# Kernel optimization log

Measured on AMD Instinct MI355X. Metric: run time of the kernel, lower is better.

## Reference

```python
import jax, jax.numpy as jnp
import numpy as np

EMB_DIM = 2048
NHEADS = 16
KVHEADS = 4
D_KQ = 128
D_V = 128


def setup_inputs() -> dict:
    key = jax.random.key(0)
    ks = jax.random.split(key, 7)
    B, S = 2, 2048
    std = 0.02
    return {
        "q": jax.random.normal(ks[0], (B, S, EMB_DIM), jnp.float32),
        "k": jax.random.normal(ks[1], (B, S, EMB_DIM), jnp.float32),
        "v": jax.random.normal(ks[2], (B, S, EMB_DIM), jnp.float32),
        # weights stored [in, out] (transposed vs torch nn.Linear storage)
        "Wq": jax.random.normal(ks[3], (EMB_DIM, NHEADS * D_KQ), jnp.float32) * std,
        "Wk": jax.random.normal(ks[4], (EMB_DIM, KVHEADS * D_KQ), jnp.float32) * std,
        "Wv": jax.random.normal(ks[5], (EMB_DIM, KVHEADS * D_V), jnp.float32) * std,
        "Wo": jax.random.normal(ks[6], (NHEADS * D_V, EMB_DIM), jnp.float32) * std,
    }


def reference(q, k, v, Wq, Wk, Wv, Wo):
    B, S, _ = q.shape
    scale = D_KQ ** -0.25  # applied to both q and k -> combined 1/sqrt(d_kq)
    # per-head projections: [B, H, S, d]
    qh = (q @ Wq).reshape(B, S, NHEADS, D_KQ).transpose(0, 2, 1, 3) * scale
    kh = (k @ Wk).reshape(B, S, KVHEADS, D_KQ).transpose(0, 2, 1, 3) * scale
    vh = (v @ Wv).reshape(B, S, KVHEADS, D_V).transpose(0, 2, 1, 3)
    # GQA expansion: each kv head repeated `expansion` times consecutively
    expansion = NHEADS // KVHEADS
    kh = jnp.repeat(kh, expansion, axis=1)  # [B, H, S, d_kq]
    vh = jnp.repeat(vh, expansion, axis=1)  # [B, H, S, d_v]
    # full softmax FIRST, then causal tril mask, then renormalize (source quirk)
    scores = jax.nn.softmax(jnp.einsum("bhqd,bhkd->bhqk", qh, kh), axis=-1)
    scores = jnp.tril(scores)  # zero out strictly-upper triangle on last 2 dims
    scores = scores / (jnp.sum(scores, axis=-1, keepdims=True) + 1e-9)
    qkv = jnp.einsum("bhqk,bhkd->bhqd", scores, vh)  # [B, H, S, d_v]
    z = qkv.transpose(0, 2, 1, 3).reshape(B, S, NHEADS * D_V)
    return z @ Wo
```

## Files before the change

### kernel.cpp

```cpp
#include <hip/hip_runtime.h>

#define S_LEN 2048
#define EMB 2048
#define NH 16
#define KVH 4
#define DH 128

typedef __bf16 bf16x8 __attribute__((ext_vector_type(8)));
typedef float floatx4 __attribute__((ext_vector_type(4)));
typedef unsigned short ushortx8 __attribute__((ext_vector_type(8)));
typedef unsigned short ushortx4 __attribute__((ext_vector_type(4)));

static __device__ __forceinline__ unsigned short f2bf(float f) {
  unsigned u = __float_as_uint(f);
  return (unsigned short)((u + 0x7fffu + ((u >> 16) & 1u)) >> 16);
}

static __device__ __forceinline__ void gload16(const unsigned short* g, unsigned short* l) {
  __builtin_amdgcn_global_load_lds(
      (const __attribute__((address_space(1))) unsigned int*)(const void*)g,
      (__attribute__((address_space(3))) unsigned int*)(void*)l, 16, 0, 0);
}

__global__ __launch_bounds__(256) void pre_kernel(
    const float* __restrict__ q, const float* __restrict__ k, const float* __restrict__ v,
    const float* __restrict__ Wq, const float* __restrict__ Wk,
    const float* __restrict__ Wv, const float* __restrict__ Wo,
    unsigned short* __restrict__ qo, unsigned short* __restrict__ ko,
    unsigned short* __restrict__ vo,
    unsigned short* __restrict__ Wqt, unsigned short* __restrict__ Wkt,
    unsigned short* __restrict__ Wvt, unsigned short* __restrict__ Wot,
    float scale) {
  __shared__ float t[32][33];
  int bx = blockIdx.x;
  if (bx < 12288) {
    const int sel = bx >> 12;
    const float* in = (sel == 0) ? q : (sel == 1) ? k : v;
    unsigned short* out = (sel == 0) ? qo : (sel == 1) ? ko : vo;
    size_t i = (((size_t)(bx & 4095)) * 256 + threadIdx.x) * 8;
    floatx4 a = *(const floatx4*)(in + i);
    floatx4 bvec = *(const floatx4*)(in + i + 4);
    ushortx8 o;
    #pragma unroll
    for (int c = 0; c < 4; ++c) { o[c] = f2bf(a[c]); o[4 + c] = f2bf(bvec[c]); }
    *(ushortx8*)(out + i) = o;
  } else {
    bx -= 12288;
    const float* W; unsigned short* Wt; int N, tile; float sc;
    if (bx < 4096)      { W = Wq; Wt = Wqt; N = 2048; tile = bx;        sc = scale; }
    else if (bx < 5120) { W = Wk; Wt = Wkt; N = 512;  tile = bx - 4096; sc = scale; }
    else if (bx < 6144) { W = Wv; Wt = Wvt; N = 512;  tile = bx - 5120; sc = 1.0f; }
    else                { W = Wo; Wt = Wot; N = 2048; tile = bx - 6144; sc = 1.0f; }
    const int ntiles = N >> 5;
    const int n0 = (tile % ntiles) * 32, k0 = (tile / ntiles) * 32;
    const int tx = threadIdx.x & 31, ty = threadIdx.x >> 5;
    #pragma unroll
    for (int r = 0; r < 4; ++r)
      t[ty + r * 8][tx] = W[(size_t)(k0 + ty + r * 8) * N + n0 + tx];
    __syncthreads();
    #pragma unroll
    for (int r = 0; r < 4; ++r)
      Wt[(size_t)(n0 + ty + r * 8) * 2048 + k0 + tx] = f2bf(t[tx][ty + r * 8] * sc);
  }
}

static __device__ __forceinline__ void gemm256_core(
    const unsigned short* __restrict__ Ab, const unsigned short* __restrict__ Bb,
    bool swap, unsigned short* As, unsigned short* Bs, floatx4 (&acc)[8][4]) {
  const int tid = threadIdx.x;
  const int lane = tid & 63, w = tid >> 6;
  const int lm = lane & 15, gq = lane >> 4;
  const int wm = w >> 2, wn = w & 3;
  const int lr = lane >> 3, lc = (lane & 7) ^ lr;

  auto stageH = [&](const unsigned short* gb, unsigned short* lt, int half, int kst) {
    #pragma unroll
    for (int qq = 0; qq < 2; ++qq) {
      const int rb = half * 128 + w * 16 + qq * 8;
      gload16(gb + (((size_t)(rb + lr)) << 11) + kst + (lc << 3), lt + rb * 64);
    }
  };

  unsigned short* As2 = As + 16384;
  unsigned short* Bs2 = Bs + 16384;

  stageH(Ab, As, 0, 0);  stageH(Ab, As, 1, 0);
  stageH(Bb, Bs, 0, 0);  stageH(Bb, Bs, 1, 0);
  stageH(Ab, As2, 0, 64);
  asm volatile("s_waitcnt vmcnt(2)" ::: "memory");
  __builtin_amdgcn_s_barrier();

  const int r1 = (wm * 128 + lm) * 64;
  const int r2 = (wn * 64 + lm) * 64;
  const int c0 = ((0 + gq) ^ (lm & 7)) * 8;
  const int c1 = ((4 + gq) ^ (lm & 7)) * 8;

#define TILE_BODY(CA, CB, OA, OB, KS1, KS2, STG1, STG4)                                         \
  {                                                                                             \
    const unsigned short* l1 = swap ? (CB) : (CA);                                              \
    const unsigned short* l2 = swap ? (CA) : (CB);                                              \
    bf16x8 op1[8], o2a[4], o2b[4];                                                              \
    _Pragma("unroll") for (int i = 0; i < 8; ++i)                                               \
      op1[i] = *(const bf16x8*)&l1[r1 + i * 1024 + c0];                                         \
    _Pragma("unroll") for (int j = 0; j < 4; ++j)                                               \
      o2a[j] = *(const bf16x8*)&l2[r2 + j * 1024 + c0];                                         \
    if (STG1) stageH(Ab, (OA), 1, (KS1));                                                       \
    __builtin_amdgcn_s_barrier();                                                               \
    asm volatile("s_waitcnt lgkmcnt(0)" ::: "memory");                                          \
    __builtin_amdgcn_s_setprio(1);                                                              \
    _Pragma("unroll") for (int i = 0; i < 8; ++i) {                                             \
      acc[i][0] = __builtin_amdgcn_mfma_f32_16x16x32_bf16(op1[i], o2a[0], acc[i][0], 0, 0, 0);  \
      acc[i][1] = __builtin_amdgcn_mfma_f32_16x16x32_bf16(op1[i], o2a[1], acc[i][1], 0, 0, 0);  \
    }                                                                                           \
    __builtin_amdgcn_s_setprio(0);                                                              \
    __builtin_amdgcn_s_barrier();                                                               \
    _Pragma("unroll") for (int j = 0; j < 4; ++j)                                               \
      o2b[j] = *(const bf16x8*)&l2[r2 + j * 1024 + c1];                                         \
    if (STG1) stageH(Bb, (OB), 0, (KS1));                                                       \
    __builtin_amdgcn_s_barrier();                                                               \
    asm volatile("s_waitcnt lgkmcnt(0)" ::: "memory");                                          \
    __builtin_amdgcn_s_setprio(1);                                                              \
    _Pragma("unroll") for (int i = 0; i < 8; ++i) {                                             \
      acc[i][2] = __builtin_amdgcn_mfma_f32_16x16x32_bf16(op1[i], o2a[2], acc[i][2], 0, 0, 0);  \
      acc[i][3] = __builtin_amdgcn_mfma_f32_16x16x32_bf16(op1[i], o2a[3], acc[i][3], 0, 0, 0);  \
    }                                                                                           \
    __builtin_amdgcn_s_setprio(0);                                                              \
    __builtin_amdgcn_s_barrier();                                                               \
    _Pragma("unroll") for (int i = 0; i < 8; ++i)                                               \
      op1[i] = *(const bf16x8*)&l1[r1 + i * 1024 + c1];                                         \
    if (STG1) stageH(Bb, (OB), 1, (KS1));                                                       \
    __builtin_amdgcn_s_barrier();                                                               \
    asm volatile("s_waitcnt lgkmcnt(0)" ::: "memory");                                          \
    __builtin_amdgcn_s_setprio(1);                                                              \
    _Pragma("unroll") for (int i = 0; i < 8; ++i) {                                             \
      acc[i][0] = __builtin_amdgcn_mfma_f32_16x16x32_bf16(op1[i], o2b[0], acc[i][0], 0, 0, 0);  \
      acc[i][1] = __builtin_amdgcn_mfma_f32_16x16x32_bf16(op1[i], o2b[1], acc[i][1], 0, 0, 0);  \
    }                                                                                           \
    __builtin_amdgcn_s_setprio(0);                                                              \
    __builtin_amdgcn_s_barrier();                                                               \
    if (STG4) stageH(Ab, (CA), 0, (KS2));                                                       \
    __builtin_amdgcn_s_barrier();                                                               \
    __builtin_amdgcn_s_setprio(1);                                                              \
    _Pragma("unroll") for (int i = 0; i < 8; ++i) {                                             \
      acc[i][2] = __builtin_amdgcn_mfma_f32_16x16x32_bf16(op1[i], o2b[2], acc[i][2], 0, 0, 0);  \
      acc[i][3] = __builtin_amdgcn_mfma_f32_16x16x32_bf16(op1[i], o2b[3], acc[i][3], 0, 0, 0);  \
    }                                                                                           \
    __builtin_amdgcn_s_setprio(0);                                                              \
    if (STG4) { asm volatile("s_waitcnt vmcnt(2)" ::: "memory"); }                              \
    else      { asm volatile("s_waitcnt vmcnt(0)" ::: "memory"); }                              \
    __builtin_amdgcn_s_barrier();                                                               \
  }

  #pragma unroll 1
  for (int t = 0; t < 30; t += 2) {
    TILE_BODY(As, Bs, As2, Bs2, (t + 1) * 64, (t + 2) * 64, 1, 1);
    TILE_BODY(As2, Bs2, As, Bs, (t + 2) * 64, (t + 3) * 64, 1, 1);
  }
  TILE_BODY(As, Bs, As2, Bs2, 31 * 64, 0, 1, 0);
  TILE_BODY(As2, Bs2, As, Bs, 0, 0, 0, 0);
#undef TILE_BODY
}

__global__ __launch_bounds__(512, 2) void proj_kernel(
    const unsigned short* __restrict__ qb, const unsigned short* __restrict__ kb,
    const unsigned short* __restrict__ vb,
    const unsigned short* __restrict__ Wqt, const unsigned short* __restrict__ Wkt,
    const unsigned short* __restrict__ Wvt,
    unsigned short* __restrict__ Qh, unsigned short* __restrict__ Kh,
    unsigned short* __restrict__ Vt) {
  extern __shared__ unsigned short lds[];
  unsigned short* As = lds;
  unsigned short* Bs = lds + 32768;
  int bid = (int)blockIdx.x;
  bid = (bid & 7) * 24 + (bid >> 3);
  const unsigned short *Ab, *Bb;
  int task, bn, bt;
  if (bid < 128)      { task = 0; bn = bid >> 4;         bt = bid & 15;         Ab = qb; Bb = Wqt; }
  else if (bid < 160) { task = 1; bn = (bid - 128) >> 4; bt = (bid - 128) & 15; Ab = kb; Bb = Wkt; }
  else                { task = 2; bn = (bid - 160) >> 4; bt = (bid - 160) & 15; Ab = vb; Bb = Wvt; }
  Ab += ((size_t)bt) << 19;
  Bb += ((size_t)bn) << 19;

  floatx4 acc[8][4] = {};
  gemm256_core(Ab, Bb, task != 2, As, Bs, acc);

  const int tid = threadIdx.x, lane = tid & 63, w = tid >> 6;
  const int lm = lane & 15, gq = lane >> 4;
  const int wm = w >> 2, wn = w & 3;
  if (task != 2) {
    unsigned short* outp = (task == 0) ? Qh : Kh;
    const int nheads = (task == 0) ? NH : KVH;
    const int head = bn * 2 + wm;
    #pragma unroll
    for (int i = 0; i < 8; ++i) {
      const int d0 = i * 16 + gq * 4;
      #pragma unroll
      for (int j = 0; j < 4; ++j) {
        const int tg = bt * 256 + wn * 64 + j * 16 + lm;
        const int b_ = tg >> 11, s_ = tg & 2047;
        ushortx4 pk;
        #pragma unroll
        for (int r = 0; r < 4; ++r) pk[r] = f2bf(acc[i][j][r]);
        *(ushortx4*)&outp[((size_t)(b_ * nheads + head) * S_LEN + s_) * DH + d0] = pk;
      }
    }
  } else {
    #pragma unroll
    for (int i = 0; i < 8; ++i) {
      const int sgl = bt * 256 + wm * 128 + i * 16 + gq * 4;
      const int b_ = sgl >> 11, s_ = sgl & 2047;
      #pragma unroll
      for (int j = 0; j < 4; ++j) {
        const int dl = wn * 64 + j * 16;
        const int head = bn * 2 + (dl >> 7);
        const int dd = (dl & 127) + lm;
        ushortx4 pk;
        #pragma unroll
        for (int r = 0; r < 4; ++r) pk[r] = f2bf(acc[i][j][r]);
        *(ushortx4*)&Vt[((size_t)(b_ * KVH + head) * DH + dd) * S_LEN + s_] = pk;
      }
    }
  }
}

__global__ __launch_bounds__(512, 2) void out_kernel(const unsigned short* __restrict__ Z,
                                                     const unsigned short* __restrict__ Wot,
                                                     float* __restrict__ outp) {
  extern __shared__ unsigned short lds[];
  unsigned short* As = lds;
  unsigned short* Bs = lds + 32768;
  int bid = (int)blockIdx.x;
  bid = (bid & 7) * 16 + (bid >> 3);
  const int bn = bid >> 4, bt = bid & 15;

  floatx4 acc[8][4] = {};
  gemm256_core(Z + (((size_t)bt) << 19), Wot + (((size_t)bn) << 19), true, As, Bs, acc);

  const int tid = threadIdx.x, lane = tid & 63, w = tid >> 6;
  const int lm = lane & 15, gq = lane >> 4;
  const int wm = w >> 2, wn = w & 3;
  #pragma unroll
  for (int i = 0; i < 8; ++i) {
    const int n0 = bn * 256 + wm * 128 + i * 16 + gq * 4;
    #pragma unroll
    for (int j = 0; j < 4; ++j) {
      const int tg = bt * 256 + wn * 64 + j * 16 + lm;
      *(floatx4*)&outp[(size_t)tg * 2048 + n0] = acc[i][j];
    }
  }
}

__global__ __launch_bounds__(256) void attn_kernel(const unsigned short* __restrict__ Qh,
                                                   const unsigned short* __restrict__ Kh,
                                                   const unsigned short* __restrict__ Vt,
                                                   unsigned short* __restrict__ Z) {
  __shared__ unsigned short Ks[64][136];
  __shared__ unsigned short Vs[128][72];
  __shared__ unsigned short Ps[4][16][88];
  const int tid = threadIdx.x;
  const int w = tid >> 6, lane = tid & 63;
  const int lm = lane & 15, gq = lane >> 4;
  const int h = blockIdx.y, b = blockIdx.z;
  const unsigned short* Kp = Kh + (size_t)(b * KVH + (h >> 2)) * S_LEN * DH;
  const unsigned short* Vp = Vt + (size_t)(b * KVH + (h >> 2)) * DH * S_LEN;

  const int krow = tid >> 2, kq4 = tid & 3;
  const int vd = tid >> 1, vhf = tid & 1;

  ushortx8 kreg[4], vreg[4];
  {
    const unsigned short* ks = Kp + (size_t)krow * DH + kq4 * 32;
    const unsigned short* vs = Vp + (size_t)vd * S_LEN + vhf * 32;
    #pragma unroll
    for (int i = 0; i < 4; ++i) { kreg[i] = *(const ushortx8*)(ks + i * 8); vreg[i] = *(const ushortx8*)(vs + i * 8); }
  }

  bf16x8 ones;
  #pragma unroll
  for (int c = 0; c < 8; ++c) ones[c] = (__bf16)1.0f;

  #pragma unroll 1
  for (int pass = 0; pass < 2; ++pass) {
    const int qt = pass ? (int)blockIdx.x : 31 - (int)blockIdx.x;
    const int Q0 = qt * 64;
    const unsigned short* Qp = Qh + ((size_t)(b * NH + h) * S_LEN + Q0) * DH;
    bf16x8 qfr[4];
    #pragma unroll
    for (int kk = 0; kk < 4; ++kk)
      qfr[kk] = *(const bf16x8*)(Qp + (size_t)(w * 16 + lm) * DH + kk * 32 + gq * 8);

    floatx4 acc_o[8] = {};
    floatx4 acc_l = {};

    for (int it = 0; it <= qt; ++it) {
      const int kv0 = it * 64;
      __syncthreads();
      #pragma unroll
      for (int i = 0; i < 4; ++i) *(ushortx8*)&Ks[krow][kq4 * 32 + i * 8] = kreg[i];
      #pragma unroll
      for (int i = 0; i < 4; ++i) *(ushortx8*)&Vs[vd][vhf * 32 + i * 8] = vreg[i];
      __syncthreads();
      if (!(pass == 1 && it == qt)) {
        const int kvn = (it < qt) ? kv0 + 64 : 0;
        const unsigned short* ks = Kp + (size_t)(kvn + krow) * DH + kq4 * 32;
        const unsigned short* vs = Vp + (size_t)vd * S_LEN + kvn + vhf * 32;
        #pragma unroll
        for (int i = 0; i < 4; ++i) { kreg[i] = *(const ushortx8*)(ks + i * 8); vreg[i] = *(const ushortx8*)(vs + i * 8); }
      }
      floatx4 sa[4] = {};
      #pragma unroll
      for (int j = 0; j < 4; ++j)
        #pragma unroll
        for (int kk = 0; kk < 4; ++kk) {
          bf16x8 bk = *(const bf16x8*)&Ks[j * 16 + lm][kk * 32 + gq * 8];
          sa[j] = __builtin_amdgcn_mfma_f32_16x16x32_bf16(qfr[kk], bk, sa[j], 0, 0, 0);
        }
      const int rowb = Q0 + w * 16 + gq * 4;
      #pragma unroll
      for (int r = 0; r < 4; ++r) {
        const int qg = rowb + r;
        #pragma unroll
        for (int j = 0; j < 4; ++j) {
          const int kg = kv0 + j * 16 + lm;
          const float p = (kg <= qg) ? __expf(sa[j][r]) : 0.0f;
          Ps[w][gq * 4 + r][j * 16 + lm] = __builtin_bit_cast(unsigned short, (__bf16)p);
        }
      }
      bf16x8 ap0 = *(const bf16x8*)&Ps[w][lm][gq * 8];
      bf16x8 ap1 = *(const bf16x8*)&Ps[w][lm][32 + gq * 8];
      #pragma unroll
      for (int jd = 0; jd < 8; ++jd) {
        bf16x8 bv0 = *(const bf16x8*)&Vs[jd * 16 + lm][gq * 8];
        bf16x8 bv1 = *(const bf16x8*)&Vs[jd * 16 + lm][32 + gq * 8];
        acc_o[jd] = __builtin_amdgcn_mfma_f32_16x16x32_bf16(bv0, ap0, acc_o[jd], 0, 0, 0);
        acc_o[jd] = __builtin_amdgcn_mfma_f32_16x16x32_bf16(bv1, ap1, acc_o[jd], 0, 0, 0);
      }
      acc_l = __builtin_amdgcn_mfma_f32_16x16x32_bf16(ones, ap0, acc_l, 0, 0, 0);
      acc_l = __builtin_amdgcn_mfma_f32_16x16x32_bf16(ones, ap1, acc_l, 0, 0, 0);
    }

    const float inv = 1.0f / acc_l[0];
    const size_t t_ = (size_t)b * S_LEN + Q0 + w * 16 + lm;
    #pragma unroll
    for (int jd = 0; jd < 8; ++jd) {
      ushortx4 pk;
      #pragma unroll
      for (int r = 0; r < 4; ++r) pk[r] = f2bf(acc_o[jd][r] * inv);
      *(ushortx4*)&Z[t_ * (NH * DH) + h * DH + jd * 16 + gq * 4] = pk;
    }
  }
}

extern "C" void kernel_launch(void* const* d_in, const int* in_sizes, int n_in,
                              void* d_out, int out_size, void* d_ws, size_t ws_size,
                              hipStream_t stream) {
  (void)in_sizes; (void)n_in; (void)out_size; (void)ws_size;
  const float* q  = (const float*)d_in[0];
  const float* k  = (const float*)d_in[1];
  const float* v  = (const float*)d_in[2];
  const float* Wq = (const float*)d_in[3];
  const float* Wk = (const float*)d_in[4];
  const float* Wv = (const float*)d_in[5];
  const float* Wo = (const float*)d_in[6];

  unsigned short* Qh  = (unsigned short*)d_ws;
  unsigned short* Kh  = Qh + (size_t)2 * NH * S_LEN * DH;
  unsigned short* Vt  = Kh + (size_t)2 * KVH * S_LEN * DH;
  unsigned short* Z   = Vt + (size_t)2 * KVH * S_LEN * DH;
  unsigned short* vb  = Z + (size_t)4096 * 2048;
  unsigned short* Wqt = vb + (size_t)4096 * 2048;
  unsigned short* Wkt = Wqt + (size_t)2048 * 2048;
  unsigned short* Wvt = Wkt + (size_t)512 * 2048;
  unsigned short* Wot = Wvt + (size_t)512 * 2048;
  unsigned short* qb = (unsigned short*)d_out;
  unsigned short* kb = qb + (size_t)4096 * 2048;

  const float scale = 0.29730177875068026f;

  static int s_attr_done = 0;
  if (!s_attr_done) {
    hipFuncSetAttribute(reinterpret_cast<const void*>(proj_kernel),
                        hipFuncAttributeMaxDynamicSharedMemorySize, 131072);
    hipFuncSetAttribute(reinterpret_cast<const void*>(out_kernel),
                        hipFuncAttributeMaxDynamicSharedMemorySize, 131072);
    s_attr_done = 1;
  }

  pre_kernel<<<22528, 256, 0, stream>>>(q, k, v, Wq, Wk, Wv, Wo,
                                        qb, kb, vb, Wqt, Wkt, Wvt, Wot, scale);
  proj_kernel<<<192, 512, 131072, stream>>>(qb, kb, vb, Wqt, Wkt, Wvt, Qh, Kh, Vt);
  attn_kernel<<<dim3(16, 16, 2), 256, 0, stream>>>(Qh, Kh, Vt, Z);
  out_kernel<<<128, 512, 131072, stream>>>(Z, Wot, (float*)d_out);
}
```

Before: 355.8 us.

## Double-buffer V via direct global-to-LDS loads and keep K fragments in registers

The attention kernel drops the K shared-memory tile and loads K fragments straight from global memory into registers in MFMA operand layout, prefetching the next tile after the QK MFMAs. V tiles are double-buffered in LDS using global_load_lds with an XOR swizzle to avoid bank conflicts. The loop now uses one barrier per iteration, with manual vmcnt waits, instead of two syncthreads around register-to-LDS copies. This aims to overlap memory traffic with compute and cut LDS round-trips, at the cost of higher register pressure (16 K vectors) and fragile hand-tuned waitcnt ordering.

```diff
diff --git a/kernel.cpp b/kernel.cpp
--- a/kernel.cpp
+++ b/kernel.cpp
@@ -254,8 +254,7 @@
                                                    const unsigned short* __restrict__ Kh,
                                                    const unsigned short* __restrict__ Vt,
                                                    unsigned short* __restrict__ Z) {
-  __shared__ unsigned short Ks[64][136];
-  __shared__ unsigned short Vs[128][72];
+  __shared__ unsigned short Vs[2][128 * 64];
   __shared__ unsigned short Ps[4][16][88];
   const int tid = threadIdx.x;
   const int w = tid >> 6, lane = tid & 63;
@@ -264,16 +263,33 @@
   const unsigned short* Kp = Kh + (size_t)(b * KVH + (h >> 2)) * S_LEN * DH;
   const unsigned short* Vp = Vt + (size_t)(b * KVH + (h >> 2)) * DH * S_LEN;
 
-  const int krow = tid >> 2, kq4 = tid & 3;
-  const int vd = tid >> 1, vhf = tid & 1;
-
-  ushortx8 kreg[4], vreg[4];
-  {
-    const unsigned short* ks = Kp + (size_t)krow * DH + kq4 * 32;
-    const unsigned short* vs = Vp + (size_t)vd * S_LEN + vhf * 32;
-    #pragma unroll
-    for (int i = 0; i < 4; ++i) { kreg[i] = *(const ushortx8*)(ks + i * 8); vreg[i] = *(const ushortx8*)(vs + i * 8); }
-  }
+  const int vrow8 = tid >> 3;
+  const int vsig = (tid & 7) ^ (vrow8 & 7);
+  const unsigned short* vsrc0 = Vp + (size_t)vrow8 * S_LEN + vsig * 8;
+
+  bf16x8 kreg[16];
+  const unsigned short* kf0 = Kp + (size_t)lm * DH + gq * 8;
+
+  auto loadV = [&](int kvn, int bsel) {
+    unsigned short* dst = &Vs[bsel][0] + w * 512;
+    #pragma unroll
+    for (int i = 0; i < 4; ++i)
+      gload16(vsrc0 + (size_t)(i * 32) * S_LEN + kvn, dst + i * 2048);
+  };
+  auto loadK = [&](int kvn) {
+    const unsigned short* kf = kf0 + (size_t)kvn * DH;
+    #pragma unroll
+    for (int j = 0; j < 4; ++j)
+      #pragma unroll
+      for (int kk = 0; kk < 4; ++kk)
+        kreg[j * 4 + kk] = *(const bf16x8*)(kf + (size_t)(j * 16) * DH + kk * 32);
+  };
+
+  int buf = 0;
+  loadV(0, 0);
+  loadK(0);
+  asm volatile("s_waitcnt vmcnt(16)" ::: "memory");
+  __builtin_amdgcn_s_barrier();
 
   bf16x8 ones;
   #pragma unroll
@@ -292,29 +308,18 @@
     floatx4 acc_o[8] = {};
     floatx4 acc_l = {};
 
+    #pragma unroll 1
     for (int it = 0; it <= qt; ++it) {
       const int kv0 = it * 64;
-      __syncthreads();
-      #pragma unroll
-      for (int i = 0; i < 4; ++i) *(ushortx8*)&Ks[krow][kq4 * 32 + i * 8] = kreg[i];
-      #pragma unroll
-      for (int i = 0; i < 4; ++i) *(ushortx8*)&Vs[vd][vhf * 32 + i * 8] = vreg[i];
-      __syncthreads();
-      if (!(pass == 1 && it == qt)) {
-        const int kvn = (it < qt) ? kv0 + 64 : 0;
-        const unsigned short* ks = Kp + (size_t)(kvn + krow) * DH + kq4 * 32;
-        const unsigned short* vs = Vp + (size_t)vd * S_LEN + kvn + vhf * 32;
-        #pragma unroll
-        for (int i = 0; i < 4; ++i) { kreg[i] = *(const ushortx8*)(ks + i * 8); vreg[i] = *(const ushortx8*)(vs + i * 8); }
-      }
+      const int kvn = (it < qt) ? kv0 + 64 : 0;
+      loadV(kvn, buf ^ 1);
       floatx4 sa[4] = {};
       #pragma unroll
       for (int j = 0; j < 4; ++j)
         #pragma unroll
-        for (int kk = 0; kk < 4; ++kk) {
-          bf16x8 bk = *(const bf16x8*)&Ks[j * 16 + lm][kk * 32 + gq * 8];
-          sa[j] = __builtin_amdgcn_mfma_f32_16x16x32_bf16(qfr[kk], bk, sa[j], 0, 0, 0);
-        }
+        for (int kk = 0; kk < 4; ++kk)
+          sa[j] = __builtin_amdgcn_mfma_f32_16x16x32_bf16(qfr[kk], kreg[j * 4 + kk], sa[j], 0, 0, 0);
+      loadK(kvn);
       const int rowb = Q0 + w * 16 + gq * 4;
       #pragma unroll
       for (int r = 0; r < 4; ++r) {
@@ -328,15 +333,22 @@
       }
       bf16x8 ap0 = *(const bf16x8*)&Ps[w][lm][gq * 8];
       bf16x8 ap1 = *(const bf16x8*)&Ps[w][lm][32 + gq * 8];
+      const unsigned short* Vb = &Vs[buf][0];
+      const int sw0 = (gq ^ (lm & 7)) * 8;
+      const int sw1 = ((4 | gq) ^ (lm & 7)) * 8;
       #pragma unroll
       for (int jd = 0; jd < 8; ++jd) {
-        bf16x8 bv0 = *(const bf16x8*)&Vs[jd * 16 + lm][gq * 8];
-        bf16x8 bv1 = *(const bf16x8*)&Vs[jd * 16 + lm][32 + gq * 8];
+        const int row = (jd * 16 + lm) * 64;
+        bf16x8 bv0 = *(const bf16x8*)&Vb[row + sw0];
+        bf16x8 bv1 = *(const bf16x8*)&Vb[row + sw1];
         acc_o[jd] = __builtin_amdgcn_mfma_f32_16x16x32_bf16(bv0, ap0, acc_o[jd], 0, 0, 0);
         acc_o[jd] = __builtin_amdgcn_mfma_f32_16x16x32_bf16(bv1, ap1, acc_o[jd], 0, 0, 0);
       }
       acc_l = __builtin_amdgcn_mfma_f32_16x16x32_bf16(ones, ap0, acc_l, 0, 0, 0);
       acc_l = __builtin_amdgcn_mfma_f32_16x16x32_bf16(ones, ap1, acc_l, 0, 0, 0);
+      asm volatile("s_waitcnt vmcnt(16) lgkmcnt(0)" ::: "memory");
+      __builtin_amdgcn_s_barrier();
+      buf ^= 1;
     }
 
     const float inv = 1.0f / acc_l[0];
```

Result: slower. 416.6 us (+17.1%).
